# Kernel tuning notes

Hardware: AMD Instinct MI355X
Metric: run time of the kernel (lower is better)

Reference implementation:

```python
import jax, jax.numpy as jnp
import numpy as np

B, T, L = 64, 60, 49
EMBED, HID, VOCAB = 768, 768, 10000


def setup_inputs() -> dict:
    key = jax.random.key(0)
    ks = jax.random.split(key, 17)
    def n(k, shape, s=1.0):
        return jax.random.normal(k, shape, dtype=jnp.float32) * s
    W = 0.02  # param init scale
    return {
        "x": n(ks[0], (B, T, 2 * EMBED)),
        "hiddens": n(ks[1], (B, T, HID)),
        "cells": n(ks[2], (B, T, HID)),
        "G": n(ks[3], (B, L, HID)),
        "H": n(ks[4], (B, L, HID)),
        # Sentinel params (bias=False)
        "W_sx": n(ks[5], (HID, 2 * EMBED), W),
        "W_sh": n(ks[6], (HID, HID), W),
        # SwitchableAttention params
        "W_ax": n(ks[7], (HID, 2 * EMBED), W),
        "W_ah": n(ks[8], (HID, HID), W),
        "W_ag": n(ks[9], (HID, HID), W),
        "w_switch": n(ks[10], (1, HID), W),
        # Atten (adaptive attention) params, bias=False
        "Wv": n(ks[11], (L, HID), W),
        "Wg": n(ks[12], (L, HID), W),
        "Ws": n(ks[13], (L, HID), W),
        "wh": n(ks[14], (1, L), W),
        # output MLP
        "W_mlp": n(ks[15], (VOCAB, HID), W),
        "b_mlp": jnp.zeros((VOCAB,), dtype=jnp.float32),
    }


def reference(x, hiddens, cells, G, H, W_sx, W_sh, W_ax, W_ah, W_ag,
              w_switch, Wv, Wg, Ws, wh, W_mlp, b_mlp):
    # Dropout layers are treated as identity (eval mode).
    b, t, _ = x.shape
    # h_{t-1}: zero initial hidden prepended, last step dropped
    h0 = jnp.zeros((b, 1, HID), dtype=hiddens.dtype)
    hiddens_t_1 = jnp.concatenate([h0, hiddens[:, :-1, :]], axis=1)

    # Sentinel gate: sigmoid(Wx x + Wh h_{t-1}) * tanh(c_t)
    gate = jax.nn.sigmoid(jnp.einsum('bte,he->bth', x, W_sx)
                          + jnp.einsum('btk,hk->bth', hiddens_t_1, W_sh))
    s_t = gate * jnp.tanh(cells)  # [B,T,HID]

    # SwitchableAttention: gate between visual H and guidance G per region,
    # conditioned on pooled word context x.
    q = jnp.einsum('bte,he->bth', x, W_ax).mean(axis=1)  # [B,HID]
    sH = jnp.einsum('blh,oh->blo', jnp.tanh(jnp.einsum('blh,kh->blk', H, W_ah) + q[:, None, :]), w_switch)  # [B,L,1]
    sG = jnp.einsum('blh,oh->blo', jnp.tanh(jnp.einsum('blh,kh->blk', G, W_ag) + q[:, None, :]), w_switch)  # [B,L,1]
    switch_weights = jax.nn.softmax(jnp.concatenate([sH, sG], axis=-1), axis=-1)  # [B,L,2]
    V = switch_weights[..., 0:1] * H + switch_weights[..., 1:2] * G  # [B,L,HID]

    # Adaptive attention (Atten): spatial attention + visual sentinel
    pv = jnp.einsum('blh,kh->blk', V, Wv)        # [B,L,49]
    pg = jnp.einsum('bth,kh->btk', hiddens, Wg)  # [B,T,49]
    z_t = jnp.einsum('btlk,ok->btlo', jnp.tanh(pv[:, None, :, :] + pg[:, :, None, :]), wh)[..., 0]  # [B,T,L]
    alpha = jax.nn.softmax(z_t, axis=-1)  # [B,T,L]
    z_s = jnp.einsum('btk,ok->bto', jnp.tanh(jnp.einsum('bth,kh->btk', s_t, Ws) + pg), wh)  # [B,T,1]
    alpha_hat = jax.nn.softmax(jnp.concatenate([z_t, z_s], axis=-1), axis=-1)  # [B,T,L+1]
    beta = alpha_hat[..., -1:]  # [B,T,1]
    c_t = jnp.einsum('btl,blh->bth', alpha, V)
    c_hat = beta * s_t + (1.0 - beta) * c_t

    scores = jnp.einsum('bth,vh->btv', c_hat + hiddens, W_mlp) + b_mlp  # [B,T,VOCAB]
    return scores, alpha, beta, switch_weights
```

## Files before the change

kernel.cpp:

```cpp
#include <hip/hip_runtime.h>

#define BB 64
#define TT 60
#define LL 49
#define HID 768
#define E2 1536
#define K2 2304
#define VOC 10000
#define BT (BB*TT)
#define BL (BB*LL)
#define NPAD_MLP 10240
#define NPAD_S 128

typedef __bf16 bf16x8 __attribute__((ext_vector_type(8)));
typedef float f32x4 __attribute__((ext_vector_type(4)));

__device__ __forceinline__ unsigned short f2bf(float f) {
  union { float f; unsigned int u; } v; v.f = f;
  unsigned int u = v.u;
  return (unsigned short)((u + 0x7fffu + ((u >> 16) & 1u)) >> 16);
}
__device__ __forceinline__ float bf2f(unsigned short h) {
  union { unsigned int u; float f; } v; v.u = ((unsigned int)h) << 16;
  return v.f;
}
__device__ __forceinline__ float fast_tanh(float x) {
  float e = __expf(2.f * x);
  return 1.f - 2.f / (e + 1.f);
}
__device__ __forceinline__ float fast_sigmoid(float x) {
  return 1.f / (1.f + __expf(-x));
}

#define NSEG 14
#define CHUNK4 2048
struct SegT {
  const float* src;
  unsigned short* dst;
  int n4;
  int rl4;
  int dstride4;
  int dcol4;
  int nrows;
  int mode;
  int blk0;
};
struct SegTable { SegT s[NSEG]; };

__global__ __launch_bounds__(256) void k_convall(SegTable tab) {
  int b = blockIdx.x;
  int si = 0;
#pragma unroll
  for (int i = 1; i < NSEG; ++i) si += (b >= tab.s[i].blk0);
  SegT sg = tab.s[si];
  int lb = b - sg.blk0;
  int end = (lb + 1) * CHUNK4; end = end < sg.n4 ? end : sg.n4;
  for (int i = lb * CHUNK4 + threadIdx.x; i < end; i += 256) {
    int row = i / sg.rl4, c = i - row * sg.rl4;
    ushort4 o; o.x = o.y = o.z = o.w = 0;
    if (sg.mode == 0) {
      float4 v = ((const float4*)sg.src)[i];
      o.x = f2bf(v.x); o.y = f2bf(v.y); o.z = f2bf(v.z); o.w = f2bf(v.w);
    } else if (sg.mode == 1) {
      if (row < sg.nrows) {
        float4 v = ((const float4*)sg.src)[i];
        o.x = f2bf(v.x); o.y = f2bf(v.y); o.z = f2bf(v.z); o.w = f2bf(v.w);
      }
    } else {
      if (row % TT != 0) {
        float4 v = ((const float4*)sg.src)[i - sg.rl4];
        o.x = f2bf(v.x); o.y = f2bf(v.y); o.z = f2bf(v.z); o.w = f2bf(v.w);
      }
    }
    ((ushort4*)sg.dst)[(size_t)row * sg.dstride4 + sg.dcol4 + c] = o;
  }
}

__global__ __launch_bounds__(256) void k_xmean(const float* __restrict__ x,
                                               unsigned short* __restrict__ xm) {
  int b = blockIdx.x / 6;
  int c = (blockIdx.x % 6) * 256 + threadIdx.x;
  float s = 0.f;
  for (int t = 0; t < TT; ++t) s += x[((size_t)b * TT + t) * E2 + c];
  xm[(size_t)b * E2 + c] = f2bf(s * (1.f / 60.f));
}

struct SSeg {
  const unsigned short* A; const unsigned short* B;
  float* C; const float* bias; const float* aux; unsigned short* outbf;
  int M, Nout, K, nMblk, blk0, emode;
};
#define NSSEG 4
struct SSegTable { SSeg s[NSSEG]; };

__global__ __launch_bounds__(256) void gemm_bt64_seg(SSegTable tab)
{
  __shared__ __attribute__((aligned(16))) unsigned short As[128*32];
  __shared__ __attribute__((aligned(16))) unsigned short Bs[64*32];
  const int tid  = threadIdx.x;
  const int lane = tid & 63;
  const int wave = tid >> 6;

  const int nwg = gridDim.x;
  const int id  = blockIdx.x;
  const int q = nwg >> 3, r = nwg & 7;
  const int xcd = id & 7, lo = id >> 3;
  const int wgid = (xcd < r ? xcd * (q + 1) : r * (q + 1) + (xcd - r) * q) + lo;

  int si = 0;
#pragma unroll
  for (int i = 1; i < NSSEG; ++i) si += (wgid >= tab.s[i].blk0);
  const SSeg sg = tab.s[si];
  const int lwg = wgid - sg.blk0;
  const int mb = lwg % sg.nMblk;
  const int nb = lwg / sg.nMblk;
  const int M = sg.M, Nout = sg.Nout, K = sg.K;
  const unsigned short* __restrict__ A  = sg.A;
  const unsigned short* __restrict__ Bw = sg.B;
  const int m0 = mb * 128;
  const int n0 = nb * 64;
  const int wm = (wave & 1) * 64;
  const int wn = (wave >> 1) * 32;

  f32x4 acc[4][2];
#pragma unroll
  for (int i = 0; i < 4; ++i)
#pragma unroll
    for (int j = 0; j < 2; ++j) acc[i][j] = f32x4{0.f, 0.f, 0.f, 0.f};

  const int lrow = lane & 15;
  const int kb   = (lane >> 4) * 8;

  for (int k0 = 0; k0 < K; k0 += 32) {
    __syncthreads();
#pragma unroll
    for (int p = 0; p < 2; ++p) {
      int slot = p * 256 + wave * 64 + lane;
      int row = slot >> 2, c8 = slot & 3;
      int ar = m0 + row; ar = ar < M ? ar : (M - 1);
      const unsigned short* asrc = A + (size_t)ar * K + k0 + c8 * 8;
      __builtin_amdgcn_global_load_lds(
          (const __attribute__((address_space(1))) void*)asrc,
          (__attribute__((address_space(3))) void*)&As[slot * 8],
          16, 0, 0);
    }
    {
      int slot = wave * 64 + lane;
      int row = slot >> 2, c8 = slot & 3;
      const unsigned short* bsrc = Bw + (size_t)(n0 + row) * K + k0 + c8 * 8;
      __builtin_amdgcn_global_load_lds(
          (const __attribute__((address_space(1))) void*)bsrc,
          (__attribute__((address_space(3))) void*)&Bs[slot * 8],
          16, 0, 0);
    }
    __syncthreads();

    bf16x8 av[4], bv[2];
#pragma unroll
    for (int i = 0; i < 4; ++i)
      av[i] = *(const bf16x8*)&As[(wm + i * 16 + lrow) * 32 + kb];
#pragma unroll
    for (int j = 0; j < 2; ++j)
      bv[j] = *(const bf16x8*)&Bs[(wn + j * 16 + lrow) * 32 + kb];
#pragma unroll
    for (int i = 0; i < 4; ++i)
#pragma unroll
      for (int j = 0; j < 2; ++j)
        acc[i][j] = __builtin_amdgcn_mfma_f32_16x16x32_bf16(av[i], bv[j], acc[i][j], 0, 0, 0);
  }

  const int cr = (lane >> 4) * 4;
  const int cc = lane & 15;
  if (sg.emode == 0) {
    float* __restrict__ C = sg.C;
    const float* __restrict__ bias = sg.bias;
#pragma unroll
    for (int i = 0; i < 4; ++i) {
      int row0 = m0 + wm + i * 16 + cr;
#pragma unroll
      for (int j = 0; j < 2; ++j) {
        int col = n0 + wn + j * 16 + cc;
        if (col < Nout) {
          float badd = bias ? bias[col] : 0.f;
#pragma unroll
          for (int r2 = 0; r2 < 4; ++r2) {
            int row = row0 + r2;
            if (row < M) C[(size_t)row * Nout + col] = acc[i][j][r2] + badd;
          }
        }
      }
    }
  } else {
    const float* __restrict__ cells = sg.aux;
    unsigned short* __restrict__ ob = sg.outbf;
#pragma unroll
    for (int i = 0; i < 4; ++i) {
      int row0 = m0 + wm + i * 16 + cr;
#pragma unroll
      for (int j = 0; j < 2; ++j) {
        int col = n0 + wn + j * 16 + cc;
        if (col < Nout) {
#pragma unroll
          for (int r2 = 0; r2 < 4; ++r2) {
            int row = row0 + r2;
            if (row < M) {
              float cv = cells[(size_t)row * Nout + col];
              ob[(size_t)row * Nout + col] = f2bf(fast_sigmoid(acc[i][j][r2]) * fast_tanh(cv));
            }
          }
        }
      }
    }
  }
}

#define BARR() do { asm volatile("" ::: "memory"); __builtin_amdgcn_s_barrier(); \
                    asm volatile("" ::: "memory"); } while (0)
#define VM2() asm volatile("s_waitcnt vmcnt(2)" ::: "memory")
#define VM0() asm volatile("s_waitcnt vmcnt(0)" ::: "memory")

#define STAGE_OP(bufi, op, kt) do {                                             \
  int k0_ = (kt) * 32;                                                          \
  _Pragma("unroll")                                                             \
  for (int l_ = 0; l_ < 2; ++l_) {                                              \
    int rr_ = l_ * 128 + sr0;                                                   \
    int ss_ = ssp ^ ((rr_ >> 1) & 3);                                           \
    int gr_ = (op) ? (n0 + rr_) : (m0 + rr_);                                   \
    const unsigned short* src_ = ((op) ? Bw : Ap) + (size_t)gr_ * K + k0_ + ss_ * 8; \
    char* dst_ = smem + (bufi) * 32768 + (op) * 16384 + l_ * 8192 + w * 1024;   \
    __builtin_amdgcn_global_load_lds(                                           \
        (const __attribute__((address_space(1))) void*)src_,                    \
        (__attribute__((address_space(3))) void*)dst_, 16, 0, 0);               \
  }                                                                             \
} while (0)

#define LDA(bufi, row) (*(const bf16x8*)(smem + (bufi) * 32768 + (row) * 64 + (cg ^ (((row) >> 1) & 3)) * 16))
#define LDB(bufi, row) (*(const bf16x8*)(smem + (bufi) * 32768 + 16384 + (row) * 64 + (cg ^ (((row) >> 1) & 3)) * 16))

#define PH0(bufi, STAGE_STMT) do {                                              \
  STAGE_STMT;                                                                   \
  bf16x8 bfr0 = LDB(bufi, wn + lrow);                                           \
  bf16x8 bfr1 = LDB(bufi, wn + 16 + lrow);                                      \
  _Pragma("unroll")                                                             \
  for (int i_ = 0; i_ < 8; ++i_) afr[i_] = LDA(bufi, wm + i_ * 16 + lrow);      \
  __builtin_amdgcn_s_setprio(1);                                                \
  _Pragma("unroll")                                                             \
  for (int i_ = 0; i_ < 8; ++i_) {                                              \
    acc[i_][0] = __builtin_amdgcn_mfma_f32_16x16x32_bf16(afr[i_], bfr0, acc[i_][0], 0, 0, 0); \
    acc[i_][1] = __builtin_amdgcn_mfma_f32_16x16x32_bf16(afr[i_], bfr1, acc[i_][1], 0, 0, 0); \
  }                                                                             \
  __builtin_amdgcn_s_setprio(0);                                                \
  BARR();                                                                       \
} while (0)

#define PH1(bufi, STAGE_STMT, VM_STMT) do {                                     \
  STAGE_STMT;                                                                   \
  bf16x8 bfr0 = LDB(bufi, wn + 32 + lrow);                                      \
  bf16x8 bfr1 = LDB(bufi, wn + 48 + lrow);                                      \
  __builtin_amdgcn_s_setprio(1);                                                \
  _Pragma("unroll")                                                             \
  for (int i_ = 0; i_ < 8; ++i_) {                                              \
    acc[i_][2] = __builtin_amdgcn_mfma_f32_16x16x32_bf16(afr[i_], bfr0, acc[i_][2], 0, 0, 0); \
    acc[i_][3] = __builtin_amdgcn_mfma_f32_16x16x32_bf16(afr[i_], bfr1, acc[i_][3], 0, 0, 0); \
  }                                                                             \
  __builtin_amdgcn_s_setprio(0);                                                \
  VM_STMT;                                                                      \
  BARR();                                                                       \
} while (0)

__global__ __launch_bounds__(512, 2) void gemm_sc(
    const unsigned short* __restrict__ Ap,
    const unsigned short* __restrict__ Bw,
    float* __restrict__ C,
    const float* __restrict__ bias,
    int M, int Nout, int K, int nMblk)
{
  extern __shared__ char smem[];
  const int tid  = threadIdx.x;
  const int lane = tid & 63;
  const int w    = tid >> 6;
  const int lrow = lane & 15;
  const int cg   = lane >> 4;
  const int sr0  = w * 16 + (lane >> 2);
  const int ssp  = lane & 3;

  const int nwg = gridDim.x;
  const int id  = blockIdx.x;
  const int q = nwg >> 3, r = nwg & 7;
  const int xcd = id & 7, lo = id >> 3;
  const int wgid = (xcd < r ? xcd * (q + 1) : r * (q + 1) + (xcd - r) * q) + lo;
  const int mb = wgid % nMblk;
  const int nb = wgid / nMblk;

  const int m0 = mb * 256;
  const int n0 = nb * 256;
  const int wm = (w >> 2) * 128;
  const int wn = (w & 3) * 64;

  f32x4 acc[8][4];
#pragma unroll
  for (int i = 0; i < 8; ++i)
#pragma unroll
    for (int j = 0; j < 4; ++j) acc[i][j] = f32x4{0.f, 0.f, 0.f, 0.f};
  bf16x8 afr[8];

  const int NT = K >> 5;

  STAGE_OP(0, 0, 0);
  STAGE_OP(0, 1, 0);
  STAGE_OP(1, 0, 1);
  VM2();
  BARR();

  for (int kt = 0; kt < NT - 2; ++kt) {
    const int c = kt & 1;
    PH0(c, STAGE_OP(c ^ 1, 1, kt + 1));
    PH1(c, STAGE_OP(c, 0, kt + 2), VM2(););
  }
  {
    const int c = (NT - 2) & 1;
    PH0(c, STAGE_OP(c ^ 1, 1, NT - 1));
    PH1(c, ;, VM0(););
  }
  {
    const int c = (NT - 1) & 1;
    PH0(c, ;);
    PH1(c, ;, ;);
  }

#pragma unroll
  for (int i = 0; i < 8; ++i) {
    int row0 = m0 + wm + i * 16 + (lane >> 4) * 4;
#pragma unroll
    for (int j = 0; j < 4; ++j) {
      int col = n0 + wn + j * 16 + (lane & 15);
      if (col < Nout) {
        float badd = bias ? bias[col] : 0.f;
#pragma unroll
        for (int r2 = 0; r2 < 4; ++r2)
          C[(size_t)(row0 + r2) * Nout + col] = acc[i][j][r2] + badd;
      }
    }
  }
}

__global__ __launch_bounds__(256) void k_switch(
    const float* __restrict__ AH, const float* __restrict__ AG,
    const float* __restrict__ q, const float* __restrict__ wsw,
    const float* __restrict__ H, const float* __restrict__ G,
    unsigned short* __restrict__ Vbf, float* __restrict__ sw_out)
{
  int bl = blockIdx.x;
  int b = bl / LL;
  int tid = threadIdx.x;
  float aH = 0.f, aG = 0.f;
  for (int h = tid; h < HID; h += 256) {
    float qv = q[b * HID + h], w = wsw[h];
    aH += fast_tanh(AH[(size_t)bl * HID + h] + qv) * w;
    aG += fast_tanh(AG[(size_t)bl * HID + h] + qv) * w;
  }
#pragma unroll
  for (int off = 32; off > 0; off >>= 1) {
    aH += __shfl_down(aH, off);
    aG += __shfl_down(aG, off);
  }
  __shared__ float redH[4], redG[4];
  int lane = tid & 63, wave = tid >> 6;
  if (lane == 0) { redH[wave] = aH; redG[wave] = aG; }
  __syncthreads();
  float sH = redH[0] + redH[1] + redH[2] + redH[3];
  float sG = redG[0] + redG[1] + redG[2] + redG[3];
  float m = fmaxf(sH, sG);
  float e0 = __expf(sH - m), e1 = __expf(sG - m);
  float inv = 1.f / (e0 + e1);
  float sw0 = e0 * inv, sw1 = e1 * inv;
  if (tid == 0) { sw_out[bl * 2] = sw0; sw_out[bl * 2 + 1] = sw1; }
  for (int h = tid; h < HID; h += 256) {
    float v = sw0 * H[(size_t)bl * HID + h] + sw1 * G[(size_t)bl * HID + h];
    Vbf[(size_t)bl * HID + h] = f2bf(v);
  }
}

__global__ __launch_bounds__(256) void k_attn(
    const float* __restrict__ PV, const float* __restrict__ PG,
    const float* __restrict__ SS, const float* __restrict__ wh,
    const unsigned short* __restrict__ stbf, const unsigned short* __restrict__ Vbf,
    const float* __restrict__ hiddens,
    float* __restrict__ alpha_out, float* __restrict__ beta_out,
    unsigned short* __restrict__ chh)
{
  const int TG = 4;
  int b  = blockIdx.x / (TT / TG);
  int t0 = (blockIdx.x % (TT / TG)) * TG;
  int tid = threadIdx.x;
  __shared__ float pg_s[TG][LL], wh_s[LL], zz[TG][LL + 1], alpha_s[TG][LL], beta_sh[TG];

  if (tid < LL) wh_s[tid] = wh[tid];
  if (tid < TG * LL) {
    int tt = tid / LL, k = tid - tt * LL;
    pg_s[tt][k] = PG[(size_t)(b * TT + t0 + tt) * 64 + k];
  }
  __syncthreads();

  if (tid < TG * (LL + 1)) {
    int tt = tid / (LL + 1), l = tid - tt * (LL + 1);
    const float* src = (l < LL) ? &PV[((size_t)b * LL + l) * 64]
                                : &SS[(size_t)(b * TT + t0 + tt) * 64];
    float acc = 0.f;
    for (int k = 0; k < LL; ++k) acc += fast_tanh(src[k] + pg_s[tt][k]) * wh_s[k];
    zz[tt][l] = acc;
  }
  __syncthreads();

  if (tid < TG) {
    int tt = tid, bt = b * TT + t0 + tt;
    float mx = -1e30f;
    for (int l = 0; l < LL; ++l) mx = fmaxf(mx, zz[tt][l]);
    float sum = 0.f;
    for (int l = 0; l < LL; ++l) { float e = __expf(zz[tt][l] - mx); alpha_s[tt][l] = e; sum += e; }
    float inv = 1.f / sum;
    for (int l = 0; l < LL; ++l) {
      alpha_s[tt][l] *= inv;
      alpha_out[(size_t)bt * LL + l] = alpha_s[tt][l];
    }
    float mx2 = fmaxf(mx, zz[tt][LL]);
    float s2 = 0.f;
    for (int l = 0; l <= LL; ++l) s2 += __expf(zz[tt][l] - mx2);
    float bet = __expf(zz[tt][LL] - mx2) / s2;
    beta_sh[tt] = bet;
    beta_out[bt] = bet;
  }
  __syncthreads();

  for (int h = tid; h < HID; h += 256) {
    float ct[TG] = {0.f, 0.f, 0.f, 0.f};
    for (int l = 0; l < LL; ++l) {
      float v = bf2f(Vbf[((size_t)b * LL + l) * HID + h]);
#pragma unroll
      for (int tt = 0; tt < TG; ++tt) ct[tt] += alpha_s[tt][l] * v;
    }
#pragma unroll
    for (int tt = 0; tt < TG; ++tt) {
      int bt = b * TT + t0 + tt;
      float bet = beta_sh[tt];
      float s = bf2f(stbf[(size_t)bt * HID + h]);
      float chat = bet * s + (1.f - bet) * ct[tt];
      chh[(size_t)bt * HID + h] = f2bf(chat + hiddens[(size_t)bt * HID + h]);
    }
  }
}

extern "C" void kernel_launch(void* const* d_in, const int* in_sizes, int n_in,
                              void* d_out, int out_size, void* d_ws, size_t ws_size,
                              hipStream_t stream)
{
  const float* x       = (const float*)d_in[0];
  const float* hiddens = (const float*)d_in[1];
  const float* cells   = (const float*)d_in[2];
  const float* G       = (const float*)d_in[3];
  const float* H       = (const float*)d_in[4];
  const float* W_sx    = (const float*)d_in[5];
  const float* W_sh    = (const float*)d_in[6];
  const float* W_ax    = (const float*)d_in[7];
  const float* W_ah    = (const float*)d_in[8];
  const float* W_ag    = (const float*)d_in[9];
  const float* w_sw    = (const float*)d_in[10];
  const float* Wv      = (const float*)d_in[11];
  const float* Wg      = (const float*)d_in[12];
  const float* Ws      = (const float*)d_in[13];
  const float* wh      = (const float*)d_in[14];
  const float* W_mlp   = (const float*)d_in[15];
  const float* b_mlp   = (const float*)d_in[16];

  float* scores = (float*)d_out;
  float* alpha  = scores + (size_t)BT * VOC;
  float* beta   = alpha + (size_t)BT * LL;
  float* swout  = beta + BT;

  char* wsp = (char*)d_ws;
  size_t off = 0;
  auto alloc = [&](size_t bytes) -> char* {
    char* p = wsp + off;
    off += (bytes + 255) & ~(size_t)255;
    return p;
  };

  unsigned short* xh     = (unsigned short*)alloc((size_t)BT * K2 * 2);
  unsigned short* wsxh   = (unsigned short*)alloc((size_t)HID * K2 * 2);
  unsigned short* waxb   = (unsigned short*)alloc((size_t)HID * E2 * 2);
  unsigned short* wahb   = (unsigned short*)alloc((size_t)HID * HID * 2);
  unsigned short* wagb   = (unsigned short*)alloc((size_t)HID * HID * 2);
  unsigned short* Hbf    = (unsigned short*)alloc((size_t)BL * HID * 2);
  unsigned short* Gbf    = (unsigned short*)alloc((size_t)BL * HID * 2);
  unsigned short* hidbf  = (unsigned short*)alloc((size_t)BT * HID * 2);
  unsigned short* wvb    = (unsigned short*)alloc((size_t)NPAD_S * HID * 2);
  unsigned short* wgb    = (unsigned short*)alloc((size_t)NPAD_S * HID * 2);
  unsigned short* wsb    = (unsigned short*)alloc((size_t)NPAD_S * HID * 2);
  unsigned short* wmlpb  = (unsigned short*)alloc((size_t)NPAD_MLP * HID * 2);
  unsigned short* Vbf    = (unsigned short*)alloc((size_t)BL * HID * 2);
  unsigned short* stbf   = (unsigned short*)alloc((size_t)BT * HID * 2);
  unsigned short* chh    = (unsigned short*)alloc((size_t)BT * HID * 2);
  unsigned short* xmbf   = (unsigned short*)alloc((size_t)BB * E2 * 2);
  float* AH = (float*)alloc((size_t)BL * HID * 4);
  float* AG = (float*)alloc((size_t)BL * HID * 4);
  float* qb = (float*)alloc((size_t)BB * HID * 4);
  float* PV = (float*)alloc((size_t)BL * 64 * 4);
  float* PG = (float*)alloc((size_t)BT * 64 * 4);
  float* SS = (float*)alloc((size_t)BT * 64 * 4);
  (void)ws_size; (void)in_sizes; (void)n_in; (void)out_size;

  SegTable tab;
  int blk = 0, si = 0;
  auto seg = [&](const float* s, unsigned short* d, int n4, int rl4, int dstride4,
                 int dcol4, int nrows, int mode) {
    tab.s[si].src = s; tab.s[si].dst = d; tab.s[si].n4 = n4; tab.s[si].rl4 = rl4;
    tab.s[si].dstride4 = dstride4; tab.s[si].dcol4 = dcol4;
    tab.s[si].nrows = nrows; tab.s[si].mode = mode; tab.s[si].blk0 = blk;
    blk += (n4 + CHUNK4 - 1) / CHUNK4; ++si;
  };
  seg(W_sx,    wsxh,  HID * 384, 384, 576, 0,   0, 0);
  seg(W_sh,    wsxh,  HID * 192, 192, 576, 384, 0, 0);
  seg(x,       xh,    BT * 384,  384, 576, 0,   0, 0);
  seg(hiddens, xh,    BT * 192,  192, 576, 384, 0, 2);
  seg(W_ax,    waxb,  HID * 384, 384, 384, 0,   0, 0);
  seg(W_ah,    wahb,  HID * 192, 192, 192, 0,   0, 0);
  seg(W_ag,    wagb,  HID * 192, 192, 192, 0,   0, 0);
  seg(H,       Hbf,   BL * 192,  192, 192, 0,   0, 0);
  seg(G,       Gbf,   BL * 192,  192, 192, 0,   0, 0);
  seg(hiddens, hidbf, BT * 192,  192, 192, 0,   0, 0);
  seg(Wv,      wvb,   NPAD_S * 192, 192, 192, 0, LL, 1);
  seg(Wg,      wgb,   NPAD_S * 192, 192, 192, 0, LL, 1);
  seg(Ws,      wsb,   NPAD_S * 192, 192, 192, 0, LL, 1);
  seg(W_mlp,   wmlpb, NPAD_MLP * 192, 192, 192, 0, VOC, 1);
  k_convall<<<blk, 256, 0, stream>>>(tab);

  k_xmean<<<BB * 6, 256, 0, stream>>>(x, xmbf);

  SSegTable mt;
  mt.s[0] = SSeg{xh,   wsxh, nullptr, nullptr, cells, stbf, BT, HID, K2,  30, 0,   1};
  mt.s[1] = SSeg{Hbf,  wahb, AH,      nullptr, nullptr, nullptr, BL, HID, HID, 25, 360, 0};
  mt.s[2] = SSeg{Gbf,  wagb, AG,      nullptr, nullptr, nullptr, BL, HID, HID, 25, 660, 0};
  mt.s[3] = SSeg{xmbf, waxb, qb,      nullptr, nullptr, nullptr, BB, HID, E2,  1,  960, 0};
  gemm_bt64_seg<<<972, 256, 0, stream>>>(mt);

  k_switch<<<BL, 256, 0, stream>>>(AH, AG, qb, w_sw, H, G, Vbf, swout);

  SSegTable st;
  st.s[0] = SSeg{Vbf,   wvb, PV, nullptr, nullptr, nullptr, BL, 64, HID, 25, 0,  0};
  st.s[1] = SSeg{hidbf, wgb, PG, nullptr, nullptr, nullptr, BT, 64, HID, 30, 25, 0};
  st.s[2] = SSeg{stbf,  wsb, SS, nullptr, nullptr, nullptr, BT, 64, HID, 30, 55, 0};
  st.s[3] = st.s[2]; st.s[3].blk0 = 0x7fffffff;
  gemm_bt64_seg<<<85, 256, 0, stream>>>(st);

  k_attn<<<BB * (TT / 4), 256, 0, stream>>>(PV, PG, SS, wh, stbf, Vbf, hiddens,
                                            alpha, beta, chh);

  gemm_sc<<<15 * 40, 512, 65536, stream>>>(chh, wmlpb, scores, b_mlp, BT, VOC, HID, 15);
}
```

Measured before the change: 304.7 us.

## Retile output GEMM to 128x256 with triple-buffered LDS; store AH/AG in bf16

Rewrites the final vocab GEMM kernel from 512-thread 256x256 tiles with double buffering to 256-thread 128x256 tiles with a three-stage LDS ring and deeper vmcnt waits, doubling the block count. The aim is better latency hiding and occupancy for the large MLP projection. Separately, the switch-attention pre-activations AH/AG are now written as bf16 through a new epilogue mode, which halves their memory traffic. The cost is slightly reduced precision in the switch logits.

```diff
diff --git a/kernel.cpp b/kernel.cpp
--- a/kernel.cpp
+++ b/kernel.cpp
@@ -37,13 +37,7 @@
 struct SegT {
   const float* src;
   unsigned short* dst;
-  int n4;
-  int rl4;
-  int dstride4;
-  int dcol4;
-  int nrows;
-  int mode;
-  int blk0;
+  int n4, rl4, dstride4, dcol4, nrows, mode, blk0;
 };
 struct SegTable { SegT s[NSEG]; };
 
@@ -190,7 +184,7 @@
         }
       }
     }
-  } else {
+  } else if (sg.emode == 1) {
     const float* __restrict__ cells = sg.aux;
     unsigned short* __restrict__ ob = sg.outbf;
 #pragma unroll
@@ -211,64 +205,79 @@
         }
       }
     }
-  }
-}
-
+  } else {
+    unsigned short* __restrict__ ob = sg.outbf;
+#pragma unroll
+    for (int i = 0; i < 4; ++i) {
+      int row0 = m0 + wm + i * 16 + cr;
+#pragma unroll
+      for (int j = 0; j < 2; ++j) {
+        int col = n0 + wn + j * 16 + cc;
+        if (col < Nout) {
+#pragma unroll
+          for (int r2 = 0; r2 < 4; ++r2) {
+            int row = row0 + r2;
+            if (row < M) ob[(size_t)row * Nout + col] = f2bf(acc[i][j][r2]);
+          }
+        }
+      }
+    }
+  }
+}
+
+#define VM6() asm volatile("s_waitcnt vmcnt(6)" ::: "memory")
+#define VM0() asm volatile("s_waitcnt vmcnt(0)" ::: "memory")
 #define BARR() do { asm volatile("" ::: "memory"); __builtin_amdgcn_s_barrier(); \
                     asm volatile("" ::: "memory"); } while (0)
-#define VM2() asm volatile("s_waitcnt vmcnt(2)" ::: "memory")
-#define VM0() asm volatile("s_waitcnt vmcnt(0)" ::: "memory")
-
-#define STAGE_OP(bufi, op, kt) do {                                             \
+
+#define SC_STAGE(bufi, kt) do {                                                 \
   int k0_ = (kt) * 32;                                                          \
   _Pragma("unroll")                                                             \
   for (int l_ = 0; l_ < 2; ++l_) {                                              \
-    int rr_ = l_ * 128 + sr0;                                                   \
-    int ss_ = ssp ^ ((rr_ >> 1) & 3);                                           \
-    int gr_ = (op) ? (n0 + rr_) : (m0 + rr_);                                   \
-    const unsigned short* src_ = ((op) ? Bw : Ap) + (size_t)gr_ * K + k0_ + ss_ * 8; \
-    char* dst_ = smem + (bufi) * 32768 + (op) * 16384 + l_ * 8192 + w * 1024;   \
+    int rr_ = l_ * 64 + wave * 16 + (lane >> 2);                                \
+    int ss_ = (lane & 3) ^ ((rr_ >> 1) & 3);                                    \
+    const unsigned short* src_ = Ap + (size_t)(m0 + rr_) * K + k0_ + ss_ * 8;   \
+    char* dst_ = smem + (bufi) * 24576 + l_ * 4096 + wave * 1024;               \
+    __builtin_amdgcn_global_load_lds(                                           \
+        (const __attribute__((address_space(1))) void*)src_,                    \
+        (__attribute__((address_space(3))) void*)dst_, 16, 0, 0);               \
+  }                                                                             \
+  _Pragma("unroll")                                                             \
+  for (int l_ = 0; l_ < 4; ++l_) {                                              \
+    int rr_ = l_ * 64 + wave * 16 + (lane >> 2);                                \
+    int ss_ = (lane & 3) ^ ((rr_ >> 1) & 3);                                    \
+    const unsigned short* src_ = Bw + (size_t)(n0 + rr_) * K + k0_ + ss_ * 8;   \
+    char* dst_ = smem + (bufi) * 24576 + 8192 + l_ * 4096 + wave * 1024;        \
     __builtin_amdgcn_global_load_lds(                                           \
         (const __attribute__((address_space(1))) void*)src_,                    \
         (__attribute__((address_space(3))) void*)dst_, 16, 0, 0);               \
   }                                                                             \
 } while (0)
 
-#define LDA(bufi, row) (*(const bf16x8*)(smem + (bufi) * 32768 + (row) * 64 + (cg ^ (((row) >> 1) & 3)) * 16))
-#define LDB(bufi, row) (*(const bf16x8*)(smem + (bufi) * 32768 + 16384 + (row) * 64 + (cg ^ (((row) >> 1) & 3)) * 16))
-
-#define PH0(bufi, STAGE_STMT) do {                                              \
+#define SC_LDA(bufi, row) (*(const bf16x8*)(smem + (bufi) * 24576 + (row) * 64 + ((cg ^ (((row) >> 1) & 3)) * 16)))
+#define SC_LDB(bufi, row) (*(const bf16x8*)(smem + (bufi) * 24576 + 8192 + (row) * 64 + ((cg ^ (((row) >> 1) & 3)) * 16)))
+
+#define SC_TILE(bufi, STAGE_STMT, VM_STMT) do {                                 \
   STAGE_STMT;                                                                   \
-  bf16x8 bfr0 = LDB(bufi, wn + lrow);                                           \
-  bf16x8 bfr1 = LDB(bufi, wn + 16 + lrow);                                      \
-  _Pragma("unroll")                                                             \
-  for (int i_ = 0; i_ < 8; ++i_) afr[i_] = LDA(bufi, wm + i_ * 16 + lrow);      \
+  bf16x8 afr0 = SC_LDA(bufi, wm + lrow);                                        \
+  bf16x8 afr1 = SC_LDA(bufi, wm + 16 + lrow);                                   \
+  bf16x8 afr2 = SC_LDA(bufi, wm + 32 + lrow);                                   \
+  bf16x8 afr3 = SC_LDA(bufi, wm + 48 + lrow);                                   \
   __builtin_amdgcn_s_setprio(1);                                                \
   _Pragma("unroll")                                                             \
-  for (int i_ = 0; i_ < 8; ++i_) {                                              \
-    acc[i_][0] = __builtin_amdgcn_mfma_f32_16x16x32_bf16(afr[i_], bfr0, acc[i_][0], 0, 0, 0); \
-    acc[i_][1] = __builtin_amdgcn_mfma_f32_16x16x32_bf16(afr[i_], bfr1, acc[i_][1], 0, 0, 0); \
-  }                                                                             \
-  __builtin_amdgcn_s_setprio(0);                                                \
-  BARR();                                                                       \
-} while (0)
-
-#define PH1(bufi, STAGE_STMT, VM_STMT) do {                                     \
-  STAGE_STMT;                                                                   \
-  bf16x8 bfr0 = LDB(bufi, wn + 32 + lrow);                                      \
-  bf16x8 bfr1 = LDB(bufi, wn + 48 + lrow);                                      \
-  __builtin_amdgcn_s_setprio(1);                                                \
-  _Pragma("unroll")                                                             \
-  for (int i_ = 0; i_ < 8; ++i_) {                                              \
-    acc[i_][2] = __builtin_amdgcn_mfma_f32_16x16x32_bf16(afr[i_], bfr0, acc[i_][2], 0, 0, 0); \
-    acc[i_][3] = __builtin_amdgcn_mfma_f32_16x16x32_bf16(afr[i_], bfr1, acc[i_][3], 0, 0, 0); \
+  for (int j_ = 0; j_ < 8; ++j_) {                                              \
+    bf16x8 b_ = SC_LDB(bufi, wn + j_ * 16 + lrow);                              \
+    acc[0][j_] = __builtin_amdgcn_mfma_f32_16x16x32_bf16(afr0, b_, acc[0][j_], 0, 0, 0); \
+    acc[1][j_] = __builtin_amdgcn_mfma_f32_16x16x32_bf16(afr1, b_, acc[1][j_], 0, 0, 0); \
+    acc[2][j_] = __builtin_amdgcn_mfma_f32_16x16x32_bf16(afr2, b_, acc[2][j_], 0, 0, 0); \
+    acc[3][j_] = __builtin_amdgcn_mfma_f32_16x16x32_bf16(afr3, b_, acc[3][j_], 0, 0, 0); \
   }                                                                             \
   __builtin_amdgcn_s_setprio(0);                                                \
   VM_STMT;                                                                      \
   BARR();                                                                       \
 } while (0)
 
-__global__ __launch_bounds__(512, 2) void gemm_sc(
+__global__ __launch_bounds__(256, 2) void gemm_sc2(
     const unsigned short* __restrict__ Ap,
     const unsigned short* __restrict__ Bw,
     float* __restrict__ C,
@@ -278,11 +287,9 @@
   extern __shared__ char smem[];
   const int tid  = threadIdx.x;
   const int lane = tid & 63;
-  const int w    = tid >> 6;
+  const int wave = tid >> 6;
   const int lrow = lane & 15;
   const int cg   = lane >> 4;
-  const int sr0  = w * 16 + (lane >> 2);
-  const int ssp  = lane & 3;
 
   const int nwg = gridDim.x;
   const int id  = blockIdx.x;
@@ -292,47 +299,39 @@
   const int mb = wgid % nMblk;
   const int nb = wgid / nMblk;
 
-  const int m0 = mb * 256;
+  const int m0 = mb * 128;
   const int n0 = nb * 256;
-  const int wm = (w >> 2) * 128;
-  const int wn = (w & 3) * 64;
-
-  f32x4 acc[8][4];
-#pragma unroll
-  for (int i = 0; i < 8; ++i)
-#pragma unroll
-    for (int j = 0; j < 4; ++j) acc[i][j] = f32x4{0.f, 0.f, 0.f, 0.f};
-  bf16x8 afr[8];
+  const int wm = (wave >> 1) * 64;
+  const int wn = (wave & 1) * 128;
+
+  f32x4 acc[4][8];
+#pragma unroll
+  for (int i = 0; i < 4; ++i)
+#pragma unroll
+    for (int j = 0; j < 8; ++j) acc[i][j] = f32x4{0.f, 0.f, 0.f, 0.f};
 
   const int NT = K >> 5;
 
-  STAGE_OP(0, 0, 0);
-  STAGE_OP(0, 1, 0);
-  STAGE_OP(1, 0, 1);
-  VM2();
+  SC_STAGE(0, 0);
+  SC_STAGE(1, 1);
+  VM6();
   BARR();
 
+  int b = 0;
   for (int kt = 0; kt < NT - 2; ++kt) {
-    const int c = kt & 1;
-    PH0(c, STAGE_OP(c ^ 1, 1, kt + 1));
-    PH1(c, STAGE_OP(c, 0, kt + 2), VM2(););
-  }
-  {
-    const int c = (NT - 2) & 1;
-    PH0(c, STAGE_OP(c ^ 1, 1, NT - 1));
-    PH1(c, ;, VM0(););
-  }
-  {
-    const int c = (NT - 1) & 1;
-    PH0(c, ;);
-    PH1(c, ;, ;);
-  }
-
-#pragma unroll
-  for (int i = 0; i < 8; ++i) {
+    int b2 = b + 2; if (b2 >= 3) b2 -= 3;
+    SC_TILE(b, SC_STAGE(b2, kt + 2), VM6(););
+    ++b; if (b == 3) b = 0;
+  }
+  SC_TILE(b, ;, VM0(););
+  ++b; if (b == 3) b = 0;
+  SC_TILE(b, ;, ;);
+
+#pragma unroll
+  for (int i = 0; i < 4; ++i) {
     int row0 = m0 + wm + i * 16 + (lane >> 4) * 4;
 #pragma unroll
-    for (int j = 0; j < 4; ++j) {
+    for (int j = 0; j < 8; ++j) {
       int col = n0 + wn + j * 16 + (lane & 15);
       if (col < Nout) {
         float badd = bias ? bias[col] : 0.f;
@@ -345,7 +344,7 @@
 }
 
 __global__ __launch_bounds__(256) void k_switch(
-    const float* __restrict__ AH, const float* __restrict__ AG,
+    const unsigned short* __restrict__ AH, const unsigned short* __restrict__ AG,
     const float* __restrict__ q, const float* __restrict__ wsw,
     const float* __restrict__ H, const float* __restrict__ G,
     unsigned short* __restrict__ Vbf, float* __restrict__ sw_out)
@@ -356,8 +355,8 @@
   float aH = 0.f, aG = 0.f;
   for (int h = tid; h < HID; h += 256) {
     float qv = q[b * HID + h], w = wsw[h];
-    aH += fast_tanh(AH[(size_t)bl * HID + h] + qv) * w;
-    aG += fast_tanh(AG[(size_t)bl * HID + h] + qv) * w;
+    aH += fast_tanh(bf2f(AH[(size_t)bl * HID + h]) + qv) * w;
+    aG += fast_tanh(bf2f(AG[(size_t)bl * HID + h]) + qv) * w;
   }
 #pragma unroll
   for (int off = 32; off > 0; off >>= 1) {
@@ -501,8 +500,8 @@
   unsigned short* stbf   = (unsigned short*)alloc((size_t)BT * HID * 2);
   unsigned short* chh    = (unsigned short*)alloc((size_t)BT * HID * 2);
   unsigned short* xmbf   = (unsigned short*)alloc((size_t)BB * E2 * 2);
-  float* AH = (float*)alloc((size_t)BL * HID * 4);
-  float* AG = (float*)alloc((size_t)BL * HID * 4);
+  unsigned short* AH     = (unsigned short*)alloc((size_t)BL * HID * 2);
+  unsigned short* AG     = (unsigned short*)alloc((size_t)BL * HID * 2);
   float* qb = (float*)alloc((size_t)BB * HID * 4);
   float* PV = (float*)alloc((size_t)BL * 64 * 4);
   float* PG = (float*)alloc((size_t)BT * 64 * 4);
@@ -538,8 +537,8 @@
 
   SSegTable mt;
   mt.s[0] = SSeg{xh,   wsxh, nullptr, nullptr, cells, stbf, BT, HID, K2,  30, 0,   1};
-  mt.s[1] = SSeg{Hbf,  wahb, AH,      nullptr, nullptr, nullptr, BL, HID, HID, 25, 360, 0};
-  mt.s[2] = SSeg{Gbf,  wagb, AG,      nullptr, nullptr, nullptr, BL, HID, HID, 25, 660, 0};
+  mt.s[1] = SSeg{Hbf,  wahb, nullptr, nullptr, nullptr, AH, BL, HID, HID, 25, 360, 2};
+  mt.s[2] = SSeg{Gbf,  wagb, nullptr, nullptr, nullptr, AG, BL, HID, HID, 25, 660, 2};
   mt.s[3] = SSeg{xmbf, waxb, qb,      nullptr, nullptr, nullptr, BB, HID, E2,  1,  960, 0};
   gemm_bt64_seg<<<972, 256, 0, stream>>>(mt);
 
@@ -555,5 +554,5 @@
   k_attn<<<BB * (TT / 4), 256, 0, stream>>>(PV, PG, SS, wh, stbf, Vbf, hiddens,
                                             alpha, beta, chh);
 
-  gemm_sc<<<15 * 40, 512, 65536, stream>>>(chh, wmlpb, scores, b_mlp, BT, VOC, HID, 15);
-}
+  gemm_sc2<<<30 * 40, 256, 73728, stream>>>(chh, wmlpb, scores, b_mlp, BT, VOC, HID, 30);
+}
```

New measurement: 300.8 us. Within noise of the previous version (-1.3%).
